# Optimization experiments

Measured on AMD Instinct MI355X. Metric: run time of the kernel, lower is better.

## Reference

```python
import jax, jax.numpy as jnp
import numpy as np

N_NODES = 50000
N_EDGES = 600000
N_DISCRETE = 70
NH = N_DISCRETE - 6          # 64
EMB = 128                    # n_embedding
D = NH + EMB                 # 192, resdnn/cross input dim
RES_HID = 512                # l_hidden entries
N_RES = 2                    # len(l_hidden)
N_CROSS = 2
PRED_HID = (2 * NH + 512) // 2  # 320
NEG_SLOPE = 0.01


def setup_inputs() -> dict:
    key = jax.random.key(0)
    ks = jax.random.split(key, 24)
    def w(k, shape, fan_in):
        return (jax.random.normal(k, shape, jnp.float32) / np.sqrt(fan_in)).astype(jnp.float32)
    inp = {
        "discrete_x": jax.random.randint(ks[0], (N_NODES, N_DISCRETE), 0, 100, jnp.int64),
        "edge_index": jax.random.randint(ks[1], (2, N_EDGES), 0, N_NODES, jnp.int64),
        # graph embedding linear + 2 GCN layers
        "w_g0": w(ks[2], (NH, EMB), NH), "b_g0": jnp.zeros((EMB,), jnp.float32),
        "w_gcn1": w(ks[3], (EMB, EMB), EMB), "b_gcn1": jnp.zeros((EMB,), jnp.float32),
        "w_gcn2": w(ks[4], (EMB, EMB), EMB), "b_gcn2": jnp.zeros((EMB,), jnp.float32),
        # ResDNN: N_RES dim-preserving residual bottleneck blocks D->RES_HID->D
        "res_w1": w(ks[5], (N_RES, D, RES_HID), D), "res_b1": jnp.zeros((N_RES, RES_HID), jnp.float32),
        "res_w2": w(ks[6], (N_RES, RES_HID, D), RES_HID), "res_b2": jnp.zeros((N_RES, D), jnp.float32),
        # CrossNet: N_CROSS layers
        "cross_w": w(ks[7], (N_CROSS, D), D), "cross_b": jnp.zeros((N_CROSS, D), jnp.float32),
        # Prediction MLP: 2D -> PRED_HID -> 1, sigmoid
        "p_w1": w(ks[8], (2 * D, PRED_HID), 2 * D), "p_b1": jnp.zeros((PRED_HID,), jnp.float32),
        "p_w2": w(ks[9], (PRED_HID, 1), PRED_HID), "p_b2": jnp.zeros((1,), jnp.float32),
    }
    return inp


def _leaky(x):
    return jax.nn.leaky_relu(x, NEG_SLOPE)


def _gcn_conv(x, W, b, row, col, n):
    # PyG GCNConv: linear, then sym-normalized aggregation over A + I, then bias
    h = x @ W
    deg = jax.ops.segment_sum(jnp.ones(row.shape, x.dtype), col, num_segments=n) + 1.0
    dinv = jax.lax.rsqrt(deg)
    norm = dinv[row] * dinv[col]            # [E]
    msg = h[row] * norm[:, None]            # [E, EMB]  (largest intermediate)
    agg = jax.ops.segment_sum(msg, col, num_segments=n)
    agg = agg + h * (dinv * dinv)[:, None]  # self-loop contribution
    return agg + b


def reference(discrete_x, edge_index, w_g0, b_g0, w_gcn1, b_gcn1, w_gcn2, b_gcn2,
              res_w1, res_b1, res_w2, res_b2, cross_w, cross_b,
              p_w1, p_b1, p_w2, p_b2):
    n = discrete_x.shape[0]
    row, col = edge_index[0], edge_index[1]
    # DiscreteFeatureEmbeddingLayer: map n_discrete_features int cols -> nh float dims
    x_d = discrete_x[:, :NH].astype(jnp.float32)
    # graph branch
    x_g = _leaky(x_d @ w_g0 + b_g0)
    x_g = _leaky(_gcn_conv(x_g, w_gcn1, b_gcn1, row, col, n))
    x_g = _leaky(_gcn_conv(x_g, w_gcn2, b_gcn2, row, col, n))
    x = jnp.concatenate([x_d, x_g], axis=-1)  # [N, D]
    # ResDNN: residual bottleneck blocks
    x_deep = x
    for i in range(N_RES):
        h = _leaky(x_deep @ res_w1[i] + res_b1[i])
        x_deep = _leaky(x_deep + h @ res_w2[i] + res_b2[i])
    # CrossNet (DCN): x_{l+1} = x0 * (x_l . w_l) + b_l + x_l
    x0 = x
    x_cross = x
    for i in range(N_CROSS):
        xw = x_cross @ cross_w[i]            # [N]
        x_cross = x0 * xw[:, None] + cross_b[i] + x_cross
    z = jnp.concatenate([x_deep, x_cross], axis=-1)  # [N, 2D]
    h = _leaky(z @ p_w1 + p_b1)
    y = jax.nn.sigmoid(h @ p_w2 + p_b2)
    return y.squeeze(-1)
```

## Files before the change

### kernel.cpp

```cpp
#include <hip/hip_runtime.h>
#include <math.h>

constexpr int NCOLS   = 70;
constexpr int NH      = 64;
constexpr int EMB     = 128;
constexpr int DD      = 192;
constexpr int RES_HID = 512;
constexpr int PRED_HID= 320;

typedef _Float16 f16x8 __attribute__((ext_vector_type(8)));
typedef float    f32x4 __attribute__((ext_vector_type(4)));
#define MFMA16F(a,b,c) __builtin_amdgcn_mfma_f32_16x16x32_f16((a),(b),(c),0,0,0)

constexpr float LO_SCALE   = 4096.0f;
constexpr float LO_DESCALE = 1.0f/4096.0f;
constexpr float Z_SCALE    = 0.0625f;
constexpr float Z_DESCALE  = 16.0f;

__device__ __forceinline__ float leaky(float x){ return x > 0.f ? x : 0.01f*x; }

__global__ void k_zero(int* p, int n){
  int i = blockIdx.x*256 + threadIdx.x;
  if (i < n) p[i] = 0;
}
__global__ void k_hist(const int* __restrict__ col, int* __restrict__ cnt, int E){
  int e = blockIdx.x*256 + threadIdx.x;
  if (e < E) atomicAdd(&cnt[col[e]], 1);
}
__global__ void k_scanA(const int* __restrict__ cnt, int* __restrict__ bsum, int n){
  __shared__ int s;
  if (threadIdx.x == 0) s = 0;
  __syncthreads();
  int i = blockIdx.x*256 + threadIdx.x;
  int v = (i < n) ? cnt[i] : 0;
  #pragma unroll
  for (int o=32;o;o>>=1) v += __shfl_xor(v, o, 64);
  if ((threadIdx.x & 63) == 0) atomicAdd(&s, v);
  __syncthreads();
  if (threadIdx.x == 0) bsum[blockIdx.x] = s;
}
__global__ void k_scanB(int* bsum, int nb){
  __shared__ int s[256];
  __shared__ int carry;
  if (threadIdx.x == 0) carry = 0;
  __syncthreads();
  for (int start = 0; start < nb; start += 256){
    int i = start + threadIdx.x;
    int v = (i < nb) ? bsum[i] : 0;
    s[threadIdx.x] = v; __syncthreads();
    for (int o=1;o<256;o<<=1){
      int t = (threadIdx.x >= o) ? s[threadIdx.x-o] : 0;
      __syncthreads();
      s[threadIdx.x] += t; __syncthreads();
    }
    if (i < nb) bsum[i] = carry + s[threadIdx.x] - v;
    __syncthreads();
    if (threadIdx.x == 255) carry += s[255];
    __syncthreads();
  }
}
__global__ void k_scanC(const int* __restrict__ cnt, const int* __restrict__ bsum,
                        int* __restrict__ base, int* __restrict__ cursor,
                        float* __restrict__ dinv, int n, int E){
  __shared__ int s[256];
  int i = blockIdx.x*256 + threadIdx.x;
  int v = (i < n) ? cnt[i] : 0;
  s[threadIdx.x] = v; __syncthreads();
  for (int o=1;o<256;o<<=1){
    int t = (threadIdx.x >= o) ? s[threadIdx.x-o] : 0;
    __syncthreads();
    s[threadIdx.x] += t; __syncthreads();
  }
  if (i < n){
    int b = bsum[blockIdx.x] + s[threadIdx.x] - v;
    base[i] = b; cursor[i] = b;
    dinv[i] = rsqrtf((float)(v + 1));
  }
  if (i == n-1) base[n] = E;
}
__global__ void k_fill(const int* __restrict__ row, const int* __restrict__ col,
                       const float* __restrict__ dinv, int* __restrict__ cursor,
                       int2* __restrict__ ebin, int E){
  int e = blockIdx.x*256 + threadIdx.x;
  if (e < E){
    int r = row[e], c = col[e];
    int slot = atomicAdd(&cursor[c], 1);
    ebin[slot] = make_int2(r, __float_as_int(dinv[r]));
  }
}

__global__ void k_wprep_pack(const float* __restrict__ W, _Float16* __restrict__ Wh,
                             _Float16* __restrict__ Wl, int K, int N){
  int idx = blockIdx.x*256 + threadIdx.x;
  if (idx < K*N){
    int k = idx / N, nn = idx - k*N;
    float v = W[idx];
    _Float16 h = (_Float16)v;
    float lo = (v - (float)h)*LO_SCALE;
    int kc = k >> 5, r = k & 31;
    int lane = (nn & 15) | ((r >> 3) << 4);
    int j = r & 7;
    size_t dst = ((size_t)((nn >> 4)*(K >> 5) + kc) << 9) + lane*8 + j;
    Wh[dst] = h;
    Wl[dst] = (_Float16)lo;
  }
}

__global__ void k_embed(const int* __restrict__ dx, float* __restrict__ A, int n){
  int idx = blockIdx.x*256 + threadIdx.x;
  if (idx < n*NH){
    int i = idx >> 6, j = idx & 63;
    A[(size_t)i*DD + j] = (float)dx[(size_t)i*NCOLS + j];
  }
}

template<int K>
__global__ void k_lin(const float* __restrict__ X, int ldx, int xoff,
                      const float* __restrict__ W, const float* __restrict__ bias,
                      float* __restrict__ out, int ldo, int ooff, int n, int act)
{
  constexpr int ST = 20;
  __shared__ __align__(16) float sxT[K*ST];
  int i0 = blockIdx.x*16;
  for (int idx = threadIdx.x; idx < 16*K; idx += 256){
    int t = idx / K, k = idx - t*K;
    int i = i0 + t;
    sxT[k*ST + t] = (i < n) ? X[(size_t)i*ldx + xoff + k] : 0.f;
  }
  __syncthreads();
  int jj = threadIdx.x & 127;
  int tg = threadIdx.x >> 7;
  float b = bias ? bias[jj] : 0.f;
  float acc[8];
  #pragma unroll
  for (int t=0;t<8;t++) acc[t] = b;
  for (int k=0;k<K;k++){
    float w = W[(size_t)k*128 + jj];
    float4 xa = *(const float4*)&sxT[k*ST + tg*8];
    float4 xb = *(const float4*)&sxT[k*ST + tg*8 + 4];
    acc[0] = fmaf(xa.x, w, acc[0]); acc[1] = fmaf(xa.y, w, acc[1]);
    acc[2] = fmaf(xa.z, w, acc[2]); acc[3] = fmaf(xa.w, w, acc[3]);
    acc[4] = fmaf(xb.x, w, acc[4]); acc[5] = fmaf(xb.y, w, acc[5]);
    acc[6] = fmaf(xb.z, w, acc[6]); acc[7] = fmaf(xb.w, w, acc[7]);
  }
  #pragma unroll
  for (int tt=0;tt<8;tt++){
    int i = i0 + tg*8 + tt;
    if (i < n){
      float v = acc[tt];
      if (act) v = leaky(v);
      out[(size_t)i*ldo + ooff + jj] = v;
    }
  }
}

__global__ void k_gather(const float* __restrict__ h, const float* __restrict__ dinv,
                         const int* __restrict__ base, const int2* __restrict__ ebin,
                         const float* __restrict__ bias, float* __restrict__ out,
                         int ldo, int ooff, int n)
{
  int node = blockIdx.x*4 + (threadIdx.x >> 6);
  int lane = threadIdx.x & 63;
  if (node >= n) return;
  int b0 = base[node], b1 = base[node+1];
  float dc = dinv[node];
  float ax = 0.f, ay = 0.f;
  int e = b0;
  for (; e + 1 < b1; e += 2){
    int2 ea = ebin[e], eb = ebin[e+1];
    float2 ha = ((const float2*)(h + (size_t)ea.x*EMB))[lane];
    float2 hb = ((const float2*)(h + (size_t)eb.x*EMB))[lane];
    float da = __int_as_float(ea.y), db = __int_as_float(eb.y);
    ax = fmaf(ha.x, da, ax); ay = fmaf(ha.y, da, ay);
    ax = fmaf(hb.x, db, ax); ay = fmaf(hb.y, db, ay);
  }
  if (e < b1){
    int2 ea = ebin[e];
    float2 ha = ((const float2*)(h + (size_t)ea.x*EMB))[lane];
    float da = __int_as_float(ea.y);
    ax = fmaf(ha.x, da, ax); ay = fmaf(ha.y, da, ay);
  }
  float2 hc = ((const float2*)(h + (size_t)node*EMB))[lane];
  float vx = leaky((ax + hc.x*dc)*dc + bias[2*lane]);
  float vy = leaky((ay + hc.y*dc)*dc + bias[2*lane+1]);
  float* op = out + (size_t)node*ldo + ooff + 2*lane;
  op[0] = vx; op[1] = vy;
}

constexpr int XS = 196;
constexpr int HS = 516;

__global__ __launch_bounds__(256,2)
void k_resblock_mfma(const float* __restrict__ X,
                     const _Float16* __restrict__ W1h, const _Float16* __restrict__ W1l,
                     const float* __restrict__ b1,
                     const _Float16* __restrict__ W2h, const _Float16* __restrict__ W2l,
                     const float* __restrict__ b2,
                     float* __restrict__ out, int n)
{
  __shared__ __align__(16) _Float16 xh[32*XS];
  __shared__ __align__(16) _Float16 xl[32*XS];
  __shared__ __align__(16) _Float16 hh[32*HS];
  int i0 = blockIdx.x*32;
  for (int idx = threadIdx.x; idx < 32*DD; idx += 256){
    int t = idx / DD, k = idx - t*DD;
    int i = i0 + t;
    float v = (i < n) ? X[(size_t)i*DD + k] : 0.f;
    _Float16 h = (_Float16)v;
    xh[t*XS + k] = h;
    xl[t*XS + k] = (_Float16)((v - (float)h)*LO_SCALE);
  }
  __syncthreads();
  int wv = threadIdx.x >> 6, ln = threadIdx.x & 63;
  int cn = ln & 15, kg = ln >> 4;
  #pragma unroll 1
  for (int ct = 0; ct < 8; ct++){
    int nt = wv*8 + ct;
    int n0 = nt*16;
    f32x4 acc0 = {0.f,0.f,0.f,0.f}, accL0 = {0.f,0.f,0.f,0.f};
    f32x4 acc1 = {0.f,0.f,0.f,0.f}, accL1 = {0.f,0.f,0.f,0.f};
    const _Float16* wbh = W1h + ((size_t)nt*6 << 9) + ln*8;
    const _Float16* wbl = W1l + ((size_t)nt*6 << 9) + ln*8;
    #pragma unroll
    for (int kc = 0; kc < 6; kc++){
      f16x8 bh = *(const f16x8*)(wbh + (kc << 9));
      f16x8 bl = *(const f16x8*)(wbl + (kc << 9));
      int k0 = kc*32 + kg*8;
      f16x8 a0h = *(const f16x8*)&xh[cn*XS + k0];
      f16x8 a0l = *(const f16x8*)&xl[cn*XS + k0];
      f16x8 a1h = *(const f16x8*)&xh[(16+cn)*XS + k0];
      f16x8 a1l = *(const f16x8*)&xl[(16+cn)*XS + k0];
      acc0  = MFMA16F(a0h, bh, acc0);
      accL0 = MFMA16F(a0l, bh, accL0);
      accL0 = MFMA16F(a0h, bl, accL0);
      acc1  = MFMA16F(a1h, bh, acc1);
      accL1 = MFMA16F(a1l, bh, accL1);
      accL1 = MFMA16F(a1h, bl, accL1);
    }
    float bb = b1[n0 + cn];
    #pragma unroll
    for (int r=0;r<4;r++){
      hh[(kg*4+r)*HS + n0 + cn]    = (_Float16)leaky(acc0[r] + accL0[r]*LO_DESCALE + bb);
      hh[(16+kg*4+r)*HS + n0 + cn] = (_Float16)leaky(acc1[r] + accL1[r]*LO_DESCALE + bb);
    }
  }
  __syncthreads();
  #pragma unroll 1
  for (int ct = 0; ct < 3; ct++){
    int nt = wv*3 + ct;
    int n0 = nt*16;
    f32x4 acc0 = {0.f,0.f,0.f,0.f}, accL0 = {0.f,0.f,0.f,0.f};
    f32x4 acc1 = {0.f,0.f,0.f,0.f}, accL1 = {0.f,0.f,0.f,0.f};
    const _Float16* wbh = W2h + ((size_t)nt*16 << 9) + ln*8;
    const _Float16* wbl = W2l + ((size_t)nt*16 << 9) + ln*8;
    #pragma unroll 4
    for (int kc = 0; kc < 16; kc++){
      f16x8 bh = *(const f16x8*)(wbh + (kc << 9));
      f16x8 bl = *(const f16x8*)(wbl + (kc << 9));
      int k0 = kc*32 + kg*8;
      f16x8 a0 = *(const f16x8*)&hh[cn*HS + k0];
      f16x8 a1 = *(const f16x8*)&hh[(16+cn)*HS + k0];
      acc0  = MFMA16F(a0, bh, acc0);
      accL0 = MFMA16F(a0, bl, accL0);
      acc1  = MFMA16F(a1, bh, acc1);
      accL1 = MFMA16F(a1, bl, accL1);
    }
    float bb = b2[n0 + cn];
    #pragma unroll
    for (int r=0;r<4;r++){
      int m0 = kg*4 + r, m1 = 16 + kg*4 + r;
      float res0 = (float)xh[m0*XS + n0 + cn] + (float)xl[m0*XS + n0 + cn]*LO_DESCALE;
      float res1 = (float)xh[m1*XS + n0 + cn] + (float)xl[m1*XS + n0 + cn]*LO_DESCALE;
      int ia = i0 + m0, ib = i0 + m1;
      if (ia < n) out[(size_t)ia*DD + n0 + cn] = leaky(res0 + acc0[r] + accL0[r]*LO_DESCALE + bb);
      if (ib < n) out[(size_t)ib*DD + n0 + cn] = leaky(res1 + acc1[r] + accL1[r]*LO_DESCALE + bb);
    }
  }
}

__global__ void k_cross(const float* __restrict__ X0, const float* __restrict__ cw,
                        const float* __restrict__ cb, float* __restrict__ out, int n)
{
  int node = blockIdx.x*4 + (threadIdx.x >> 6);
  int lane = threadIdx.x & 63;
  if (node >= n) return;
  const float* xr = X0 + (size_t)node*DD;
  float v0[3], xc[3];
  #pragma unroll
  for (int m=0;m<3;m++){ v0[m] = xr[lane + 64*m]; xc[m] = v0[m]; }
  #pragma unroll
  for (int l=0;l<2;l++){
    float p = 0.f;
    #pragma unroll
    for (int m=0;m<3;m++) p += xc[m]*cw[l*DD + lane + 64*m];
    #pragma unroll
    for (int off=32; off>0; off>>=1) p += __shfl_xor(p, off, 64);
    #pragma unroll
    for (int m=0;m<3;m++) xc[m] = v0[m]*p + cb[l*DD + lane + 64*m] + xc[m];
  }
  #pragma unroll
  for (int m=0;m<3;m++) out[(size_t)node*DD + lane + 64*m] = xc[m];
}

constexpr int ZS = 392;

__global__ __launch_bounds__(256,3)
void k_pred_mfma(const float* __restrict__ deep, const float* __restrict__ cross,
                 const _Float16* __restrict__ Wh, const _Float16* __restrict__ Wl,
                 const float* __restrict__ b1,
                 const float* __restrict__ w2, const float* __restrict__ b2,
                 float* __restrict__ y, int n)
{
  __shared__ __align__(16) _Float16 zh[32*ZS];
  __shared__ __align__(16) _Float16 zl[32*ZS];
  __shared__ float sred[4][32];
  int i0 = blockIdx.x*32;
  for (int idx = threadIdx.x; idx < 32*2*DD; idx += 256){
    int t = idx / (2*DD), k = idx - t*(2*DD);
    int i = i0 + t;
    float v = 0.f;
    if (i < n) v = (k < DD) ? deep[(size_t)i*DD + k] : cross[(size_t)i*DD + (k - DD)];
    v *= Z_SCALE;
    _Float16 h = (_Float16)v;
    float lo = (v - (float)h)*LO_SCALE;
    zh[t*ZS + k] = h;
    zl[t*ZS + k] = (_Float16)lo;
  }
  __syncthreads();
  int wv = threadIdx.x >> 6, ln = threadIdx.x & 63;
  int cn = ln & 15, kg = ln >> 4;
  float vs0[4] = {0.f,0.f,0.f,0.f};
  float vs1[4] = {0.f,0.f,0.f,0.f};
  #pragma unroll 1
  for (int ct = 0; ct < 5; ct++){
    int nt = wv*5 + ct;
    int n0 = nt*16;
    f32x4 acc0 = {0.f,0.f,0.f,0.f}, accL0 = {0.f,0.f,0.f,0.f};
    f32x4 acc1 = {0.f,0.f,0.f,0.f}, accL1 = {0.f,0.f,0.f,0.f};
    const _Float16* wbh = Wh + ((size_t)nt*12 << 9) + ln*8;
    const _Float16* wbl = Wl + ((size_t)nt*12 << 9) + ln*8;
    #pragma unroll 4
    for (int kc = 0; kc < 12; kc++){
      f16x8 bh = *(const f16x8*)(wbh + (kc << 9));
      f16x8 bl = *(const f16x8*)(wbl + (kc << 9));
      int k0 = kc*32 + kg*8;
      f16x8 a0h = *(const f16x8*)&zh[cn*ZS + k0];
      f16x8 a0l = *(const f16x8*)&zl[cn*ZS + k0];
      f16x8 a1h = *(const f16x8*)&zh[(16+cn)*ZS + k0];
      f16x8 a1l = *(const f16x8*)&zl[(16+cn)*ZS + k0];
      acc0  = MFMA16F(a0h, bh, acc0);
      accL0 = MFMA16F(a0l, bh, accL0);
      accL0 = MFMA16F(a0h, bl, accL0);
      acc1  = MFMA16F(a1h, bh, acc1);
      accL1 = MFMA16F(a1l, bh, accL1);
      accL1 = MFMA16F(a1h, bl, accL1);
    }
    float bb = b1[n0 + cn];
    float ww = w2[n0 + cn];
    #pragma unroll
    for (int r=0;r<4;r++){
      float v0 = (acc0[r] + accL0[r]*LO_DESCALE)*Z_DESCALE + bb;
      float v1 = (acc1[r] + accL1[r]*LO_DESCALE)*Z_DESCALE + bb;
      vs0[r] += leaky(v0)*ww;
      vs1[r] += leaky(v1)*ww;
    }
  }
  #pragma unroll
  for (int r=0;r<4;r++){
    #pragma unroll
    for (int off=1; off<16; off<<=1){
      vs0[r] += __shfl_xor(vs0[r], off, 64);
      vs1[r] += __shfl_xor(vs1[r], off, 64);
    }
  }
  if (cn == 0){
    #pragma unroll
    for (int r=0;r<4;r++){
      sred[wv][kg*4 + r]      = vs0[r];
      sred[wv][16 + kg*4 + r] = vs1[r];
    }
  }
  __syncthreads();
  if (threadIdx.x < 32){
    int m = threadIdx.x;
    float s = sred[0][m] + sred[1][m] + sred[2][m] + sred[3][m] + b2[0];
    int i = i0 + m;
    if (i < n) y[i] = 1.f/(1.f + expf(-s));
  }
}

extern "C" void kernel_launch(void* const* d_in, const int* in_sizes, int n_in,
                              void* d_out, int out_size, void* d_ws, size_t ws_size,
                              hipStream_t stream)
{
  const int*   dx      = (const int*)d_in[0];
  const int*   ei      = (const int*)d_in[1];
  const float* w_g0    = (const float*)d_in[2];
  const float* b_g0    = (const float*)d_in[3];
  const float* w_gcn1  = (const float*)d_in[4];
  const float* b_gcn1  = (const float*)d_in[5];
  const float* w_gcn2  = (const float*)d_in[6];
  const float* b_gcn2  = (const float*)d_in[7];
  const float* res_w1  = (const float*)d_in[8];
  const float* res_b1  = (const float*)d_in[9];
  const float* res_w2  = (const float*)d_in[10];
  const float* res_b2  = (const float*)d_in[11];
  const float* cross_w = (const float*)d_in[12];
  const float* cross_b = (const float*)d_in[13];
  const float* p_w1    = (const float*)d_in[14];
  const float* p_b1    = (const float*)d_in[15];
  const float* p_w2    = (const float*)d_in[16];
  const float* p_b2    = (const float*)d_in[17];
  float* y = (float*)d_out;

  int n = in_sizes[0] / NCOLS;
  int E = in_sizes[1] / 2;
  const int* row = ei;
  const int* col = ei + E;

  float* ws  = (float*)d_ws;
  float* A   = ws;
  float* B   = A  + (size_t)192*n;
  float* G   = B  + (size_t)192*n;
  float* E1  = G;
  float* E2v = G  + (size_t)128*n;
  float* Dx  = G;
  float* dinv= G  + (size_t)256*n;
  int*  cnt    = (int*)(dinv + n);
  int*  base   = cnt + n;
  int*  cursor = base + n + 2;
  int*  bsum   = cursor + n;
  int2* ebin   = (int2*)((((uintptr_t)(bsum + 256)) + 15) & ~(uintptr_t)15);
  _Float16* wt1h = (_Float16*)((((uintptr_t)(ebin + E)) + 15) & ~(uintptr_t)15);
  _Float16* wt1l = wt1h + (size_t)2*RES_HID*DD;
  _Float16* wt2h = wt1l + (size_t)2*RES_HID*DD;
  _Float16* wt2l = wt2h + (size_t)2*RES_HID*DD;
  _Float16* wph  = wt2l + (size_t)2*RES_HID*DD;
  _Float16* wpl  = wph  + (size_t)PRED_HID*2*DD;

  dim3 blk(256);
  int nb = (n + 255)/256;

  {
    int sz = DD*RES_HID;
    k_wprep_pack<<<(sz+255)/256, blk, 0, stream>>>(res_w1,       wt1h,       wt1l,       DD, RES_HID);
    k_wprep_pack<<<(sz+255)/256, blk, 0, stream>>>(res_w1 + sz,  wt1h + sz,  wt1l + sz,  DD, RES_HID);
    k_wprep_pack<<<(sz+255)/256, blk, 0, stream>>>(res_w2,       wt2h,       wt2l,       RES_HID, DD);
    k_wprep_pack<<<(sz+255)/256, blk, 0, stream>>>(res_w2 + sz,  wt2h + sz,  wt2l + sz,  RES_HID, DD);
    int pz = 2*DD*PRED_HID;
    k_wprep_pack<<<(pz+255)/256, blk, 0, stream>>>(p_w1, wph, wpl, 2*DD, PRED_HID);
  }

  k_zero <<<nb, blk, 0, stream>>>(cnt, n);
  k_hist <<<(E+255)/256, blk, 0, stream>>>(col, cnt, E);
  k_scanA<<<nb, blk, 0, stream>>>(cnt, bsum, n);
  k_scanB<<<1, blk, 0, stream>>>(bsum, nb);
  k_scanC<<<nb, blk, 0, stream>>>(cnt, bsum, base, cursor, dinv, n, E);
  k_fill <<<(E+255)/256, blk, 0, stream>>>(row, col, dinv, cursor, ebin, E);

  k_embed<<<(n*NH+255)/256, blk, 0, stream>>>(dx, A, n);
  k_lin<64> <<<(n+15)/16, blk, 0, stream>>>(A, DD, 0, w_g0, b_g0, E1, EMB, 0, n, 1);
  k_lin<128><<<(n+15)/16, blk, 0, stream>>>(E1, EMB, 0, w_gcn1, nullptr, E2v, EMB, 0, n, 0);
  k_gather  <<<(n+3)/4,   blk, 0, stream>>>(E2v, dinv, base, ebin, b_gcn1, E1, EMB, 0, n);
  k_lin<128><<<(n+15)/16, blk, 0, stream>>>(E1, EMB, 0, w_gcn2, nullptr, E2v, EMB, 0, n, 0);
  k_gather  <<<(n+3)/4,   blk, 0, stream>>>(E2v, dinv, base, ebin, b_gcn2, A, DD, NH, n);
  int rbt = (n + 31)/32;
  k_resblock_mfma<<<rbt, blk, 0, stream>>>(A, wt1h, wt1l, res_b1,
                                           wt2h, wt2l, res_b2, B, n);
  k_resblock_mfma<<<rbt, blk, 0, stream>>>(B, wt1h + (size_t)DD*RES_HID, wt1l + (size_t)DD*RES_HID,
                                           res_b1 + RES_HID,
                                           wt2h + (size_t)DD*RES_HID, wt2l + (size_t)DD*RES_HID,
                                           res_b2 + DD, B, n);
  k_cross<<<(n+3)/4, blk, 0, stream>>>(A, cross_w, cross_b, Dx, n);
  k_pred_mfma<<<rbt, blk, 0, stream>>>(B, Dx, wph, wpl, p_b1, p_w2, p_b2, y, n);
}
```

Baseline: 707.9 us.

## Register-cache A fragments and software-prefetch weight tiles in ResDNN block kernel

In the first GEMM of the residual block, the A fragments (hi/lo split of X) are now loaded from LDS into registers once instead of once per column tile. The weight fragments for the next column tile are prefetched from global memory while the current tile's MFMAs run. The second GEMM is reorganised so that all three column tiles share each k-step's A load from shared memory, with next-k weights double-buffered in registers. The aim is to hide global weight-load latency and cut redundant LDS reads, at the cost of much higher VGPR pressure and possibly lower occupancy.

```diff
diff --git a/kernel.cpp b/kernel.cpp
--- a/kernel.cpp
+++ b/kernel.cpp
@@ -213,67 +213,118 @@
   __syncthreads();
   int wv = threadIdx.x >> 6, ln = threadIdx.x & 63;
   int cn = ln & 15, kg = ln >> 4;
-  #pragma unroll 1
-  for (int ct = 0; ct < 8; ct++){
-    int nt = wv*8 + ct;
-    int n0 = nt*16;
-    f32x4 acc0 = {0.f,0.f,0.f,0.f}, accL0 = {0.f,0.f,0.f,0.f};
-    f32x4 acc1 = {0.f,0.f,0.f,0.f}, accL1 = {0.f,0.f,0.f,0.f};
-    const _Float16* wbh = W1h + ((size_t)nt*6 << 9) + ln*8;
-    const _Float16* wbl = W1l + ((size_t)nt*6 << 9) + ln*8;
-    #pragma unroll
-    for (int kc = 0; kc < 6; kc++){
-      f16x8 bh = *(const f16x8*)(wbh + (kc << 9));
-      f16x8 bl = *(const f16x8*)(wbl + (kc << 9));
+
+  {
+    f16x8 A0h[6], A0l[6], A1h[6], A1l[6];
+    #pragma unroll
+    for (int kc=0;kc<6;kc++){
       int k0 = kc*32 + kg*8;
-      f16x8 a0h = *(const f16x8*)&xh[cn*XS + k0];
-      f16x8 a0l = *(const f16x8*)&xl[cn*XS + k0];
-      f16x8 a1h = *(const f16x8*)&xh[(16+cn)*XS + k0];
-      f16x8 a1l = *(const f16x8*)&xl[(16+cn)*XS + k0];
-      acc0  = MFMA16F(a0h, bh, acc0);
-      accL0 = MFMA16F(a0l, bh, accL0);
-      accL0 = MFMA16F(a0h, bl, accL0);
-      acc1  = MFMA16F(a1h, bh, acc1);
-      accL1 = MFMA16F(a1l, bh, accL1);
-      accL1 = MFMA16F(a1h, bl, accL1);
-    }
-    float bb = b1[n0 + cn];
-    #pragma unroll
-    for (int r=0;r<4;r++){
-      hh[(kg*4+r)*HS + n0 + cn]    = (_Float16)leaky(acc0[r] + accL0[r]*LO_DESCALE + bb);
-      hh[(16+kg*4+r)*HS + n0 + cn] = (_Float16)leaky(acc1[r] + accL1[r]*LO_DESCALE + bb);
-    }
-  }
-  __syncthreads();
-  #pragma unroll 1
-  for (int ct = 0; ct < 3; ct++){
-    int nt = wv*3 + ct;
-    int n0 = nt*16;
-    f32x4 acc0 = {0.f,0.f,0.f,0.f}, accL0 = {0.f,0.f,0.f,0.f};
-    f32x4 acc1 = {0.f,0.f,0.f,0.f}, accL1 = {0.f,0.f,0.f,0.f};
-    const _Float16* wbh = W2h + ((size_t)nt*16 << 9) + ln*8;
-    const _Float16* wbl = W2l + ((size_t)nt*16 << 9) + ln*8;
-    #pragma unroll 4
-    for (int kc = 0; kc < 16; kc++){
-      f16x8 bh = *(const f16x8*)(wbh + (kc << 9));
-      f16x8 bl = *(const f16x8*)(wbl + (kc << 9));
+      A0h[kc] = *(const f16x8*)&xh[cn*XS + k0];
+      A0l[kc] = *(const f16x8*)&xl[cn*XS + k0];
+      A1h[kc] = *(const f16x8*)&xh[(16+cn)*XS + k0];
+      A1l[kc] = *(const f16x8*)&xl[(16+cn)*XS + k0];
+    }
+    float bias1[8];
+    #pragma unroll
+    for (int ct=0;ct<8;ct++) bias1[ct] = b1[(wv*8+ct)*16 + cn];
+    const _Float16* pbh = W1h + ((size_t)(wv*8)*6 << 9) + ln*8;
+    const _Float16* pbl = W1l + ((size_t)(wv*8)*6 << 9) + ln*8;
+    f16x8 Bh[6], Bl[6];
+    #pragma unroll
+    for (int kc=0;kc<6;kc++){
+      Bh[kc] = *(const f16x8*)(pbh + ((size_t)kc<<9));
+      Bl[kc] = *(const f16x8*)(pbl + ((size_t)kc<<9));
+    }
+    #pragma unroll 1
+    for (int ct = 0; ct < 8; ct++){
+      f16x8 Bh2[6], Bl2[6];
+      if (ct < 7){
+        const _Float16* nh = pbh + ((size_t)((ct+1)*6) << 9);
+        const _Float16* nl = pbl + ((size_t)((ct+1)*6) << 9);
+        #pragma unroll
+        for (int kc=0;kc<6;kc++){
+          Bh2[kc] = *(const f16x8*)(nh + ((size_t)kc<<9));
+          Bl2[kc] = *(const f16x8*)(nl + ((size_t)kc<<9));
+        }
+      }
+      f32x4 acc0={0.f,0.f,0.f,0.f}, accL0={0.f,0.f,0.f,0.f};
+      f32x4 acc1={0.f,0.f,0.f,0.f}, accL1={0.f,0.f,0.f,0.f};
+      #pragma unroll
+      for (int kc=0;kc<6;kc++){
+        acc0  = MFMA16F(A0h[kc], Bh[kc], acc0);
+        accL0 = MFMA16F(A0l[kc], Bh[kc], accL0);
+        accL0 = MFMA16F(A0h[kc], Bl[kc], accL0);
+        acc1  = MFMA16F(A1h[kc], Bh[kc], acc1);
+        accL1 = MFMA16F(A1l[kc], Bh[kc], accL1);
+        accL1 = MFMA16F(A1h[kc], Bl[kc], accL1);
+      }
+      int n0 = (wv*8+ct)*16;
+      float bb = bias1[ct];
+      #pragma unroll
+      for (int r=0;r<4;r++){
+        hh[(kg*4+r)*HS + n0 + cn]    = (_Float16)leaky(acc0[r] + accL0[r]*LO_DESCALE + bb);
+        hh[(16+kg*4+r)*HS + n0 + cn] = (_Float16)leaky(acc1[r] + accL1[r]*LO_DESCALE + bb);
+      }
+      #pragma unroll
+      for (int kc=0;kc<6;kc++){ Bh[kc]=Bh2[kc]; Bl[kc]=Bl2[kc]; }
+    }
+  }
+  __syncthreads();
+
+  {
+    f32x4 acc[3][2], accL[3][2];
+    #pragma unroll
+    for (int c=0;c<3;c++){
+      #pragma unroll
+      for (int g=0;g<2;g++){
+        acc[c][g]  = (f32x4){0.f,0.f,0.f,0.f};
+        accL[c][g] = (f32x4){0.f,0.f,0.f,0.f};
+      }
+    }
+    f16x8 B2h[3], B2l[3];
+    #pragma unroll
+    for (int c=0;c<3;c++){
+      size_t off = ((size_t)((wv*3+c)*16) << 9) + ln*8;
+      B2h[c] = *(const f16x8*)(W2h + off);
+      B2l[c] = *(const f16x8*)(W2l + off);
+    }
+    #pragma unroll 1
+    for (int kc=0;kc<16;kc++){
+      f16x8 N2h[3], N2l[3];
+      if (kc < 15){
+        #pragma unroll
+        for (int c=0;c<3;c++){
+          size_t off = ((size_t)((wv*3+c)*16 + kc + 1) << 9) + ln*8;
+          N2h[c] = *(const f16x8*)(W2h + off);
+          N2l[c] = *(const f16x8*)(W2l + off);
+        }
+      }
       int k0 = kc*32 + kg*8;
       f16x8 a0 = *(const f16x8*)&hh[cn*HS + k0];
       f16x8 a1 = *(const f16x8*)&hh[(16+cn)*HS + k0];
-      acc0  = MFMA16F(a0, bh, acc0);
-      accL0 = MFMA16F(a0, bl, accL0);
-      acc1  = MFMA16F(a1, bh, acc1);
-      accL1 = MFMA16F(a1, bl, accL1);
-    }
-    float bb = b2[n0 + cn];
-    #pragma unroll
-    for (int r=0;r<4;r++){
-      int m0 = kg*4 + r, m1 = 16 + kg*4 + r;
-      float res0 = (float)xh[m0*XS + n0 + cn] + (float)xl[m0*XS + n0 + cn]*LO_DESCALE;
-      float res1 = (float)xh[m1*XS + n0 + cn] + (float)xl[m1*XS + n0 + cn]*LO_DESCALE;
-      int ia = i0 + m0, ib = i0 + m1;
-      if (ia < n) out[(size_t)ia*DD + n0 + cn] = leaky(res0 + acc0[r] + accL0[r]*LO_DESCALE + bb);
-      if (ib < n) out[(size_t)ib*DD + n0 + cn] = leaky(res1 + acc1[r] + accL1[r]*LO_DESCALE + bb);
+      #pragma unroll
+      for (int c=0;c<3;c++){
+        acc[c][0]  = MFMA16F(a0, B2h[c], acc[c][0]);
+        accL[c][0] = MFMA16F(a0, B2l[c], accL[c][0]);
+        acc[c][1]  = MFMA16F(a1, B2h[c], acc[c][1]);
+        accL[c][1] = MFMA16F(a1, B2l[c], accL[c][1]);
+      }
+      #pragma unroll
+      for (int c=0;c<3;c++){ B2h[c]=N2h[c]; B2l[c]=N2l[c]; }
+    }
+    #pragma unroll
+    for (int c=0;c<3;c++){
+      int n0 = (wv*3+c)*16;
+      float bb = b2[n0 + cn];
+      #pragma unroll
+      for (int r=0;r<4;r++){
+        int m0 = kg*4 + r, m1 = 16 + kg*4 + r;
+        float res0 = (float)xh[m0*XS + n0 + cn] + (float)xl[m0*XS + n0 + cn]*LO_DESCALE;
+        float res1 = (float)xh[m1*XS + n0 + cn] + (float)xl[m1*XS + n0 + cn]*LO_DESCALE;
+        int ia = i0 + m0, ib = i0 + m1;
+        if (ia < n) out[(size_t)ia*DD + n0 + cn] = leaky(res0 + acc[c][0][r] + accL[c][0][r]*LO_DESCALE + bb);
+        if (ib < n) out[(size_t)ib*DD + n0 + cn] = leaky(res1 + acc[c][1][r] + accL[c][1][r]*LO_DESCALE + bb);
+      }
     }
   }
 }
```

New measurement: 684.8 us. 1.03x faster.
